# Performance work log

Hardware: AMD Instinct MI355X
Metric: run time of the kernel (lower is better)

Reference implementation:

```python
import jax, jax.numpy as jnp
import numpy as np

B, S, DM, H = 4, 4096, 1024, 16
HD = DM // H  # 64


def setup_inputs() -> dict:
    key = jax.random.key(0)
    ks = jax.random.split(key, 9)
    sc = 0.02
    x = jax.random.normal(ks[0], (B, S, DM), dtype=jnp.float32)
    Wq = jax.random.normal(ks[1], (DM, DM), dtype=jnp.float32) * sc
    bq = jnp.zeros((DM,), dtype=jnp.float32)
    Wk = jax.random.normal(ks[2], (DM, HD), dtype=jnp.float32) * sc
    bk = jnp.zeros((HD,), dtype=jnp.float32)
    Wv = jax.random.normal(ks[3], (DM, HD), dtype=jnp.float32) * sc
    bv = jnp.zeros((HD,), dtype=jnp.float32)
    Wo = jax.random.normal(ks[4], (DM, DM), dtype=jnp.float32) * sc
    bo = jnp.zeros((DM,), dtype=jnp.float32)
    return {"x": x, "Wq": Wq, "bq": bq, "Wk": Wk, "bk": bk,
            "Wv": Wv, "bv": bv, "Wo": Wo, "bo": bo}


def reference(x, Wq, bq, Wk, bk, Wv, bv, Wo, bo):
    b, s, _ = x.shape
    q = (x @ Wq + bq).reshape(b, s, H, HD)          # [B,S,H,D]
    k = (x @ Wk + bk)                                # [B,S,D] (single KV head)
    v = (x @ Wv + bv)                                # [B,S,D]
    # Faithful to source: k/v expanded over head axis, matmul over last two
    # dims of [B,S,H,D] -> scores are per-token head-vs-head: [B,S,H,H].
    k_e = jnp.broadcast_to(k[:, :, None, :], (b, s, H, HD))
    v_e = jnp.broadcast_to(v[:, :, None, :], (b, s, H, HD))
    scores = jnp.einsum('bshd,bsgd->bshg', q, k_e) / jnp.sqrt(jnp.float32(HD))
    attn = jax.nn.softmax(scores, axis=-1)           # uniform (scores const over g)
    out = jnp.einsum('bshg,bsgd->bshd', attn, v_e)   # [B,S,H,D]
    return out.reshape(b, s, DM) @ Wo + bo
```

## Files before the change

kernel.cpp:

```cpp
#include <hip/hip_runtime.h>

#define M_TOTAL 16384
#define DMODEL  1024
#define HDIM    64
#define NHEAD   16

typedef _Float16 half8 __attribute__((ext_vector_type(8)));
typedef float    f32x4 __attribute__((ext_vector_type(4)));
typedef float    f32x2 __attribute__((ext_vector_type(2)));

__global__ __launch_bounds__(256) void prep_kernel(const float* __restrict__ Wv,
                                                   const float* __restrict__ Wo,
                                                   _Float16* __restrict__ WvT,
                                                   _Float16* __restrict__ WosumT) {
    const int t = blockIdx.x * 256 + threadIdx.x;
    {
        const int d = t & 63, k = t >> 6;
        WvT[d * DMODEL + k] = (_Float16)Wv[k * HDIM + d];
    }
    {
        const int n = t & 1023, d = t >> 10;
        float s = 0.f;
        #pragma unroll
        for (int h = 0; h < NHEAD; ++h) s += Wo[(h * HDIM + d) * DMODEL + n];
        WosumT[n * HDIM + d] = (_Float16)s;
    }
}

#define VP_S 68

__global__ __launch_bounds__(512, 4) void vproj_kernel(const float* __restrict__ X,
                                                       const float* __restrict__ bv,
                                                       const _Float16* __restrict__ WvT,
                                                       _Float16* __restrict__ V) {
    __shared__ float Vp[8][16][VP_S];

    const int tid = threadIdx.x;
    const int l   = tid & 63;
    const int w   = tid >> 6;
    const int lr  = l & 15;
    const int lk  = l >> 4;
    const int m0  = blockIdx.x * 16;
    const int k0  = w * 128;

    const float* xp = X + (size_t)(m0 + lr) * DMODEL + k0 + lk * 8;
    f32x4 xb[8];
    #pragma unroll
    for (int s = 0; s < 4; ++s) {
        xb[2 * s]     = *(const f32x4*)(xp + s * 32);
        xb[2 * s + 1] = *(const f32x4*)(xp + s * 32 + 4);
    }
    half8 Bf[4][4];
    #pragma unroll
    for (int n4 = 0; n4 < 4; ++n4)
        #pragma unroll
        for (int s = 0; s < 4; ++s)
            Bf[n4][s] = *(const half8*)&WvT[(size_t)(n4 * 16 + lr) * DMODEL + k0 + s * 32 + lk * 8];

    f32x4 acc[4] = {};
    #pragma unroll
    for (int s = 0; s < 4; ++s) {
        union { _Float16 h[8]; half8 v; } pk;
        #pragma unroll
        for (int j = 0; j < 4; ++j) {
            pk.h[j]     = (_Float16)xb[2 * s][j];
            pk.h[4 + j] = (_Float16)xb[2 * s + 1][j];
        }
        #pragma unroll
        for (int n4 = 0; n4 < 4; ++n4)
            acc[n4] = __builtin_amdgcn_mfma_f32_16x16x32_f16(pk.v, Bf[n4][s], acc[n4], 0, 0, 0);
    }
    #pragma unroll
    for (int n4 = 0; n4 < 4; ++n4)
        #pragma unroll
        for (int j = 0; j < 4; ++j)
            Vp[w][lk * 4 + j][n4 * 16 + lr] = acc[n4][j];
    __syncthreads();

    const int idx = tid * 2;
    const int r   = idx >> 6;
    const int c   = idx & 63;
    f32x2 s2 = {};
    #pragma unroll
    for (int p = 0; p < 8; ++p) s2 += *(const f32x2*)&Vp[p][r][c];
    s2 += *(const f32x2*)&bv[c];
    union { _Float16 h[2]; unsigned int u; } o;
    o.h[0] = (_Float16)s2[0];
    o.h[1] = (_Float16)s2[1];
    *(unsigned int*)&V[(size_t)(m0 + r) * HDIM + c] = o.u;
}

__global__ __launch_bounds__(256, 8) void oproj_kernel(const _Float16* __restrict__ V,
                                                       const float* __restrict__ bo,
                                                       const _Float16* __restrict__ WosumT,
                                                       float* __restrict__ Out) {
    const int tid = threadIdx.x;
    const int l   = tid & 63;
    const int w   = tid >> 6;
    const int lr  = l & 15;
    const int lk  = l >> 4;
    const int m0  = (blockIdx.x >> 1) * 16;
    const int nb  = (blockIdx.x & 1) * 512 + w * 128;

    const _Float16* vp = V + (size_t)(m0 + lr) * HDIM + lk * 8;
    const half8 a0 = *(const half8*)vp;
    const half8 a1 = *(const half8*)(vp + 32);

    const _Float16* wb = &WosumT[(size_t)(nb + lr) * HDIM];
    half8 b0 = *(const half8*)(wb + lk * 8);
    half8 b1 = *(const half8*)(wb + 32 + lk * 8);

    #pragma unroll
    for (int g = 0; g < 8; ++g) {
        const half8 c0 = b0, c1 = b1;
        if (g < 7) {
            const _Float16* wn = wb + (size_t)(g + 1) * 16 * HDIM;
            b0 = *(const half8*)(wn + lk * 8);
            b1 = *(const half8*)(wn + 32 + lk * 8);
        }
        f32x4 o = {};
        o = __builtin_amdgcn_mfma_f32_16x16x32_f16(a0, c0, o, 0, 0, 0);
        o = __builtin_amdgcn_mfma_f32_16x16x32_f16(a1, c1, o, 0, 0, 0);
        const int n0 = nb + g * 16;
        const float bov = bo[n0 + lr];
        #pragma unroll
        for (int j = 0; j < 4; ++j)
            Out[(size_t)(m0 + lk * 4 + j) * DMODEL + n0 + lr] = o[j] + bov;
    }
}

extern "C" void kernel_launch(void* const* d_in, const int* in_sizes, int n_in,
                              void* d_out, int out_size, void* d_ws, size_t ws_size,
                              hipStream_t stream) {
    const float* x  = (const float*)d_in[0];
    const float* Wv = (const float*)d_in[5];
    const float* bv = (const float*)d_in[6];
    const float* Wo = (const float*)d_in[7];
    const float* bo = (const float*)d_in[8];

    _Float16* WvT    = (_Float16*)d_ws;
    _Float16* WosumT = (_Float16*)((char*)d_ws + 64 * 1024 * 2);
    _Float16* V      = (_Float16*)((char*)d_ws + 256 * 1024);
    float*    out    = (float*)d_out;

    prep_kernel<<<256, 256, 0, stream>>>(Wv, Wo, WvT, WosumT);
    vproj_kernel<<<M_TOTAL / 16, 512, 0, stream>>>(x, bv, WvT, V);
    oproj_kernel<<<2048, 256, 0, stream>>>(V, bo, WosumT, out);
}
```

Measured before the change: 61.64 us.

## Stage oproj output through LDS for coalesced 16-byte row stores

The output projection now writes its MFMA results into a padded shared-memory tile and then stores full rows with 16-byte vector writes, replacing the strided 4-byte scattered stores. Each block covers all 1024 columns for 16 rows, so the grid is halved and each wave handles 256 columns in two halves, preloading 8 B-fragments at a time. The goal is better store coalescing on the 64 MB fp32 output write. The cost is more registers and LDS per block, which lowers occupancy (launch bound drops from 8 to 4).

```diff
diff --git a/kernel.cpp b/kernel.cpp
--- a/kernel.cpp
+++ b/kernel.cpp
@@ -90,42 +90,54 @@
     *(unsigned int*)&V[(size_t)(m0 + r) * HDIM + c] = o.u;
 }
 
-__global__ __launch_bounds__(256, 8) void oproj_kernel(const _Float16* __restrict__ V,
+#define OB_S 132
+
+__global__ __launch_bounds__(256, 4) void oproj_kernel(const _Float16* __restrict__ V,
                                                        const float* __restrict__ bo,
                                                        const _Float16* __restrict__ WosumT,
                                                        float* __restrict__ Out) {
+    __shared__ float Ob[4][16][OB_S];
+
     const int tid = threadIdx.x;
     const int l   = tid & 63;
     const int w   = tid >> 6;
     const int lr  = l & 15;
     const int lk  = l >> 4;
-    const int m0  = (blockIdx.x >> 1) * 16;
-    const int nb  = (blockIdx.x & 1) * 512 + w * 128;
+    const int m0  = blockIdx.x * 16;
 
     const _Float16* vp = V + (size_t)(m0 + lr) * HDIM + lk * 8;
     const half8 a0 = *(const half8*)vp;
     const half8 a1 = *(const half8*)(vp + 32);
 
-    const _Float16* wb = &WosumT[(size_t)(nb + lr) * HDIM];
-    half8 b0 = *(const half8*)(wb + lk * 8);
-    half8 b1 = *(const half8*)(wb + 32 + lk * 8);
+    const int rs = l >> 5;
+    const int ck = l & 31;
 
     #pragma unroll
-    for (int g = 0; g < 8; ++g) {
-        const half8 c0 = b0, c1 = b1;
-        if (g < 7) {
-            const _Float16* wn = wb + (size_t)(g + 1) * 16 * HDIM;
-            b0 = *(const half8*)(wn + lk * 8);
-            b1 = *(const half8*)(wn + 32 + lk * 8);
+    for (int h = 0; h < 2; ++h) {
+        const int cb = w * 256 + h * 128;
+        half8 Bf[8][2];
+        #pragma unroll
+        for (int t = 0; t < 8; ++t) {
+            const _Float16* wb = &WosumT[(size_t)(cb + t * 16 + lr) * HDIM];
+            Bf[t][0] = *(const half8*)(wb + lk * 8);
+            Bf[t][1] = *(const half8*)(wb + 32 + lk * 8);
         }
-        f32x4 o = {};
-        o = __builtin_amdgcn_mfma_f32_16x16x32_f16(a0, c0, o, 0, 0, 0);
-        o = __builtin_amdgcn_mfma_f32_16x16x32_f16(a1, c1, o, 0, 0, 0);
-        const int n0 = nb + g * 16;
-        const float bov = bo[n0 + lr];
         #pragma unroll
-        for (int j = 0; j < 4; ++j)
-            Out[(size_t)(m0 + lk * 4 + j) * DMODEL + n0 + lr] = o[j] + bov;
+        for (int t = 0; t < 8; ++t) {
+            f32x4 o = {};
+            o = __builtin_amdgcn_mfma_f32_16x16x32_f16(a0, Bf[t][0], o, 0, 0, 0);
+            o = __builtin_amdgcn_mfma_f32_16x16x32_f16(a1, Bf[t][1], o, 0, 0, 0);
+            const float bov = bo[cb + t * 16 + lr];
+            #pragma unroll
+            for (int j = 0; j < 4; ++j)
+                Ob[w][lk * 4 + j][t * 16 + lr] = o[j] + bov;
+        }
+        #pragma unroll
+        for (int i = 0; i < 8; ++i) {
+            const int r = i * 2 + rs;
+            const f32x4 v4 = *(const f32x4*)&Ob[w][r][ck * 4];
+            *(f32x4*)&Out[(size_t)(m0 + r) * DMODEL + cb + ck * 4] = v4;
+        }
     }
 }
 
@@ -145,5 +157,5 @@
 
     prep_kernel<<<256, 256, 0, stream>>>(Wv, Wo, WvT, WosumT);
     vproj_kernel<<<M_TOTAL / 16, 512, 0, stream>>>(x, bv, WvT, V);
-    oproj_kernel<<<2048, 256, 0, stream>>>(V, bo, WosumT, out);
+    oproj_kernel<<<M_TOTAL / 16, 256, 0, stream>>>(V, bo, WosumT, out);
 }
```

Result: faster. 55.76 us (-9.5%).
